# Optimization experiments

Measured on AMD Instinct MI355X. Metric: run time of the kernel, lower is better.

Reference implementation:

```python
import jax, jax.numpy as jnp
import numpy as np

B, N, D, H, C = 4, 512, 128, 128, 3


def setup_inputs() -> dict:
    key = jax.random.key(0)
    k1, k2, k3, k4, k5 = jax.random.split(key, 5)
    s1 = 1.0 / np.sqrt(2 * D)  # torch Linear default init scale (uniform bound); randn is fine for a numerics baseline
    s2 = 1.0 / np.sqrt(H)
    return {
        "h_dense": jax.random.normal(k1, (B, N, D), dtype=jnp.float32),
        "W1": jax.random.normal(k2, (H, 2 * D), dtype=jnp.float32) * s1,
        "b1": jax.random.normal(k3, (H,), dtype=jnp.float32) * s1,
        "W2": jax.random.normal(k4, (C, H), dtype=jnp.float32) * s2,
        "b2": jax.random.normal(k5, (C,), dtype=jnp.float32) * s2,
    }


def reference(h_dense, W1, b1, W2, b2):
    # Linear(concat(h_src, h_dst)) == h_src @ W1[:, :D].T + h_dst @ W1[:, D:].T + b1
    # which avoids materializing the (B, N, N, 2D) concat tensor (same math).
    d = h_dense.shape[-1]
    a = jnp.einsum("bnd,hd->bnh", h_dense, W1[:, :d])  # src projection (B, N, H)
    b = jnp.einsum("bnd,hd->bnh", h_dense, W1[:, d:])  # dst projection (B, N, H)
    pre = a[:, :, None, :] + b[:, None, :, :] + b1      # (B, N, N, H)
    act = jax.nn.silu(pre)
    logits = jnp.einsum("bijh,ch->bijc", act, W2) + b2  # (B, N, N, C)
    # symmetrize over the pair axes (dropout is identity in eval mode)
    return (logits + jnp.swapaxes(logits, 1, 2)) * 0.5
```

## Files before the change

### kernel.cpp

```cpp
#include <hip/hip_runtime.h>
#include <hip/hip_fp16.h>

#define B_ 4
#define N_ 512
#define D_ 128
#define H_ 128
#define C_ 3

#define NEG_LOG2E   (-1.4426950408889634f)
#define NEG_HALF_LN2 (-0.34657359027997264f)

#define PH   4
#define PHH  32
#define TROW 40

typedef _Float16 half8  __attribute__((ext_vector_type(8)));
typedef _Float16 half4v __attribute__((ext_vector_type(4)));

__device__ __forceinline__ float exp2_fast(float x) {
    return __builtin_amdgcn_exp2f(x);
}

__global__ __launch_bounds__(256) void proj_gemm(
    const float* __restrict__ hd, const float* __restrict__ W1,
    const float* __restrict__ b1, _Float16* __restrict__ At, _Float16* __restrict__ Bt)
{
    __shared__ float hsT[64][36];
    __shared__ float wt [64][68];
    const int m0      = blockIdx.x * 32;
    const int by      = blockIdx.y;
    const int halfSel = by >> 1;
    const int wrow0   = (by & 1) * 64;

    const int t  = threadIdx.x;
    const int r  = t >> 4, c4 = t & 15;
    const int tx = t & 15, ty = t >> 4;

    float acc[2][4] = {};

    for (int kc = 0; kc < 2; ++kc) {
        if (kc) __syncthreads();
        #pragma unroll
        for (int i = 0; i < 2; ++i) {
            const int m = r + 16 * i;
            float4 v = *(const float4*)&hd[(m0 + m) * D_ + kc * 64 + 4 * c4];
            hsT[4 * c4 + 0][m] = v.x; hsT[4 * c4 + 1][m] = v.y;
            hsT[4 * c4 + 2][m] = v.z; hsT[4 * c4 + 3][m] = v.w;
        }
        #pragma unroll
        for (int i = 0; i < 4; ++i) {
            const int o = r + 16 * i;
            float4 v = *(const float4*)&W1[(wrow0 + o) * (2 * D_) + halfSel * D_ + kc * 64 + 4 * c4];
            wt[4 * c4 + 0][o] = v.x; wt[4 * c4 + 1][o] = v.y;
            wt[4 * c4 + 2][o] = v.z; wt[4 * c4 + 3][o] = v.w;
        }
        __syncthreads();
        #pragma unroll 8
        for (int k = 0; k < 64; ++k) {
            float2 a  = *(const float2*)&hsT[k][2 * ty];
            float4 bv = *(const float4*)&wt [k][4 * tx];
            acc[0][0] = fmaf(a.x, bv.x, acc[0][0]); acc[0][1] = fmaf(a.x, bv.y, acc[0][1]);
            acc[0][2] = fmaf(a.x, bv.z, acc[0][2]); acc[0][3] = fmaf(a.x, bv.w, acc[0][3]);
            acc[1][0] = fmaf(a.y, bv.x, acc[1][0]); acc[1][1] = fmaf(a.y, bv.y, acc[1][1]);
            acc[1][2] = fmaf(a.y, bv.z, acc[1][2]); acc[1][3] = fmaf(a.y, bv.w, acc[1][3]);
        }
    }

    _Float16* dst = halfSel ? Bt : At;
    const int ocol = wrow0 + 4 * tx;
    float4 bias = make_float4(0.f, 0.f, 0.f, 0.f);
    if (!halfSel) bias = *(const float4*)&b1[ocol];
    #pragma unroll
    for (int i = 0; i < 2; ++i) {
        half4v o;
        o[0] = (_Float16)((acc[i][0] + bias.x) * NEG_LOG2E);
        o[1] = (_Float16)((acc[i][1] + bias.y) * NEG_LOG2E);
        o[2] = (_Float16)((acc[i][2] + bias.z) * NEG_LOG2E);
        o[3] = (_Float16)((acc[i][3] + bias.w) * NEG_LOG2E);
        *(half4v*)&dst[(m0 + 2 * ty + i) * H_ + ocol] = o;
    }
}

__global__ __launch_bounds__(256, 3) void pair_kernel(
    const _Float16* __restrict__ At, const _Float16* __restrict__ Bt,
    const float* __restrict__ W2, const float* __restrict__ b2,
    float* __restrict__ out)
{
    __shared__ __align__(16) _Float16 tiles[8][32 * TROW];
    const int T = N_ / 32;
    int tp = blockIdx.x;
    const int b = blockIdx.y;
    int I = 0;
    while (tp >= T - I) { tp -= T - I; ++I; }
    const int J = I + tp;

    const int tid = threadIdx.x;
    const int stile = tid >> 6;
    const int lane  = tid & 63;
    const int srow  = lane >> 1;
    const int scp   = lane & 1;
    const _Float16* gsrc = ((stile & 2) ? Bt : At)
        + (size_t)(b * N_ + ((stile & 1) ? J : I) * 32 + srow) * H_;
    _Float16* ybase = &tiles[stile][srow * TROW];
    _Float16* ebase = &tiles[stile + 4][srow * TROW];

    const int ti = tid >> 4, tj = tid & 15;
    float acc[4][3] = {};

    for (int ph = 0; ph < PH; ++ph) {
        if (ph) __syncthreads();
        #pragma unroll
        for (int q = 0; q < 2; ++q) {
            const int c = scp * 2 + q;
            half8 yv = *(const half8*)&gsrc[ph * PHH + c * 8];
            half8 ev;
            #pragma unroll
            for (int e = 0; e < 8; ++e)
                ev[e] = (_Float16)exp2_fast((float)yv[e]);
            *(half8*)&ybase[c * 8] = yv;
            *(half8*)&ebase[c * 8] = ev;
        }
        __syncthreads();

        #pragma unroll 2
        for (int c = 0; c < 4; ++c) {
            const int oI0 =  ti       * TROW + c * 8;
            const int oI1 = (ti + 16) * TROW + c * 8;
            const int oJ0 =  tj       * TROW + c * 8;
            const int oJ1 = (tj + 16) * TROW + c * 8;
            half8 yAI0 = *(const half8*)&tiles[0][oI0], yAI1 = *(const half8*)&tiles[0][oI1];
            half8 yAJ0 = *(const half8*)&tiles[1][oJ0], yAJ1 = *(const half8*)&tiles[1][oJ1];
            half8 yBI0 = *(const half8*)&tiles[2][oI0], yBI1 = *(const half8*)&tiles[2][oI1];
            half8 yBJ0 = *(const half8*)&tiles[3][oJ0], yBJ1 = *(const half8*)&tiles[3][oJ1];
            half8 eAI0 = *(const half8*)&tiles[4][oI0], eAI1 = *(const half8*)&tiles[4][oI1];
            half8 eAJ0 = *(const half8*)&tiles[5][oJ0], eAJ1 = *(const half8*)&tiles[5][oJ1];
            half8 eBI0 = *(const half8*)&tiles[6][oI0], eBI1 = *(const half8*)&tiles[6][oI1];
            half8 eBJ0 = *(const half8*)&tiles[7][oJ0], eBJ1 = *(const half8*)&tiles[7][oJ1];

            const int hb = ph * PHH + c * 8;
            float4 w0a = *(const float4*)&W2[hb],          w0b = *(const float4*)&W2[hb + 4];
            float4 w1a = *(const float4*)&W2[H_ + hb],     w1b = *(const float4*)&W2[H_ + hb + 4];
            float4 w2a = *(const float4*)&W2[2 * H_ + hb], w2b = *(const float4*)&W2[2 * H_ + hb + 4];
            const float w0[8] = {w0a.x, w0a.y, w0a.z, w0a.w, w0b.x, w0b.y, w0b.z, w0b.w};
            const float w1[8] = {w1a.x, w1a.y, w1a.z, w1a.w, w1b.x, w1b.y, w1b.z, w1b.w};
            const float w2[8] = {w2a.x, w2a.y, w2a.z, w2a.w, w2b.x, w2b.y, w2b.z, w2b.w};

            #define SILU4(p, yAIv, yBIv, eAIv, eBIv, yAJv, yBJv, eAJv, eBJv)      \
            {                                                                     \
                half8 y1 = (yAIv) + (yBJv);                                       \
                half8 y2 = (yAJv) + (yBIv);                                       \
                half8 e1 = (eAIv) * (eBJv);                                       \
                half8 e2 = (eAJv) * (eBIv);                                       \
                half8 d1 = e1 + (_Float16)1.0f;                                   \
                half8 d2 = e2 + (_Float16)1.0f;                                   \
                half8 pp = d1 * d2;                                               \
                half8 num = y1 * d2 + y2 * d1;                                    \
                _Pragma("unroll")                                                 \
                for (int e = 0; e < 8; ++e) {                                     \
                    const float s = (float)num[e]                                 \
                                  * __builtin_amdgcn_rcpf((float)pp[e]);          \
                    acc[p][0] = fmaf(s, w0[e], acc[p][0]);                        \
                    acc[p][1] = fmaf(s, w1[e], acc[p][1]);                        \
                    acc[p][2] = fmaf(s, w2[e], acc[p][2]);                        \
                }                                                                 \
            }
            SILU4(0, yAI0, yBI0, eAI0, eBI0, yAJ0, yBJ0, eAJ0, eBJ0)
            SILU4(1, yAI0, yBI0, eAI0, eBI0, yAJ1, yBJ1, eAJ1, eBJ1)
            SILU4(2, yAI1, yBI1, eAI1, eBI1, yAJ0, yBJ0, eAJ0, eBJ0)
            SILU4(3, yAI1, yBI1, eAI1, eBI1, yAJ1, yBJ1, eAJ1, eBJ1)
            #undef SILU4
        }
    }

    const float b20 = b2[0], b21 = b2[1], b22 = b2[2];
    #pragma unroll
    for (int p = 0; p < 4; ++p) {
        const int i = I * 32 + ti + (p >> 1) * 16;
        const int j = J * 32 + tj + (p & 1) * 16;
        const float o0 = fmaf(NEG_HALF_LN2, acc[p][0], b20);
        const float o1 = fmaf(NEG_HALF_LN2, acc[p][1], b21);
        const float o2 = fmaf(NEG_HALF_LN2, acc[p][2], b22);
        float* p1 = out + ((size_t)(b * N_ + i) * N_ + j) * C_;
        float* p2 = out + ((size_t)(b * N_ + j) * N_ + i) * C_;
        p1[0] = o0; p1[1] = o1; p1[2] = o2;
        p2[0] = o0; p2[1] = o1; p2[2] = o2;
    }
}

extern "C" void kernel_launch(void* const* d_in, const int* in_sizes, int n_in,
                              void* d_out, int out_size, void* d_ws, size_t ws_size,
                              hipStream_t stream) {
    const float* hd = (const float*)d_in[0];
    const float* W1 = (const float*)d_in[1];
    const float* b1 = (const float*)d_in[2];
    const float* W2 = (const float*)d_in[3];
    const float* b2 = (const float*)d_in[4];
    float* out = (float*)d_out;

    _Float16* At = (_Float16*)d_ws;
    _Float16* Bt = At + B_ * N_ * H_;

    proj_gemm<<<dim3((B_ * N_) / 32, 4), dim3(256), 0, stream>>>(hd, W1, b1, At, Bt);

    const int T = N_ / 32;
    pair_kernel<<<dim3(T * (T + 1) / 2, B_), dim3(256), 0, stream>>>(At, Bt, W2, b2, out);
}
```

Before: 48.00 us.

## Halve pair tile height to 16x32 and double block count

```diff
diff --git a/kernel.cpp b/kernel.cpp
--- a/kernel.cpp
+++ b/kernel.cpp
@@ -12,7 +12,7 @@
 
 #define PH   4
 #define PHH  32
-#define TROW 40
+#define SROW 40
 
 typedef _Float16 half8  __attribute__((ext_vector_type(8)));
 typedef _Float16 half4v __attribute__((ext_vector_type(4)));
@@ -86,56 +86,54 @@
     const float* __restrict__ W2, const float* __restrict__ b2,
     float* __restrict__ out)
 {
-    __shared__ __align__(16) _Float16 tiles[8][32 * TROW];
-    const int T = N_ / 32;
+    __shared__ __align__(16) _Float16 yt[96 * SROW];
+    __shared__ __align__(16) _Float16 et[96 * SROW];
+
+    const int b = blockIdx.y;
     int tp = blockIdx.x;
-    const int b = blockIdx.y;
-    int I = 0;
-    while (tp >= T - I) { tp -= T - I; ++I; }
-    const int J = I + tp;
+    int jt = 0;
+    while (tp >= 2 * jt + 2) { tp -= 2 * jt + 2; ++jt; }
+    const int it = tp;
+    const int I0 = it * 16, J0 = jt * 32;
 
     const int tid = threadIdx.x;
-    const int stile = tid >> 6;
-    const int lane  = tid & 63;
-    const int srow  = lane >> 1;
-    const int scp   = lane & 1;
-    const _Float16* gsrc = ((stile & 2) ? Bt : At)
-        + (size_t)(b * N_ + ((stile & 1) ? J : I) * 32 + srow) * H_;
-    _Float16* ybase = &tiles[stile][srow * TROW];
-    _Float16* ebase = &tiles[stile + 4][srow * TROW];
-
     const int ti = tid >> 4, tj = tid & 15;
-    float acc[4][3] = {};
+
+    float acc[2][3] = {};
 
     for (int ph = 0; ph < PH; ++ph) {
         if (ph) __syncthreads();
-        #pragma unroll
-        for (int q = 0; q < 2; ++q) {
-            const int c = scp * 2 + q;
-            half8 yv = *(const half8*)&gsrc[ph * PHH + c * 8];
+        for (int u = tid; u < 384; u += 256) {
+            const int row = u >> 2, c = u & 3;
+            const _Float16* base;
+            int gr;
+            if (row < 32)      { base = (row < 16) ? At : Bt; gr = I0 + (row & 15); }
+            else if (row < 64) { base = At; gr = J0 + (row - 32); }
+            else               { base = Bt; gr = J0 + (row - 64); }
+            half8 yv = *(const half8*)&base[(size_t)(b * N_ + gr) * H_ + ph * PHH + c * 8];
             half8 ev;
             #pragma unroll
             for (int e = 0; e < 8; ++e)
                 ev[e] = (_Float16)exp2_fast((float)yv[e]);
-            *(half8*)&ybase[c * 8] = yv;
-            *(half8*)&ebase[c * 8] = ev;
+            *(half8*)&yt[row * SROW + c * 8] = yv;
+            *(half8*)&et[row * SROW + c * 8] = ev;
         }
         __syncthreads();
 
         #pragma unroll 2
         for (int c = 0; c < 4; ++c) {
-            const int oI0 =  ti       * TROW + c * 8;
-            const int oI1 = (ti + 16) * TROW + c * 8;
-            const int oJ0 =  tj       * TROW + c * 8;
-            const int oJ1 = (tj + 16) * TROW + c * 8;
-            half8 yAI0 = *(const half8*)&tiles[0][oI0], yAI1 = *(const half8*)&tiles[0][oI1];
-            half8 yAJ0 = *(const half8*)&tiles[1][oJ0], yAJ1 = *(const half8*)&tiles[1][oJ1];
-            half8 yBI0 = *(const half8*)&tiles[2][oI0], yBI1 = *(const half8*)&tiles[2][oI1];
-            half8 yBJ0 = *(const half8*)&tiles[3][oJ0], yBJ1 = *(const half8*)&tiles[3][oJ1];
-            half8 eAI0 = *(const half8*)&tiles[4][oI0], eAI1 = *(const half8*)&tiles[4][oI1];
-            half8 eAJ0 = *(const half8*)&tiles[5][oJ0], eAJ1 = *(const half8*)&tiles[5][oJ1];
-            half8 eBI0 = *(const half8*)&tiles[6][oI0], eBI1 = *(const half8*)&tiles[6][oI1];
-            half8 eBJ0 = *(const half8*)&tiles[7][oJ0], eBJ1 = *(const half8*)&tiles[7][oJ1];
+            const int oAi  = ( 0 + ti) * SROW + c * 8;
+            const int oBi  = (16 + ti) * SROW + c * 8;
+            const int oAj0 = (32 + tj) * SROW + c * 8;
+            const int oAj1 = (48 + tj) * SROW + c * 8;
+            const int oBj0 = (64 + tj) * SROW + c * 8;
+            const int oBj1 = (80 + tj) * SROW + c * 8;
+            half8 yAi  = *(const half8*)&yt[oAi],  eAi  = *(const half8*)&et[oAi];
+            half8 yBi  = *(const half8*)&yt[oBi],  eBi  = *(const half8*)&et[oBi];
+            half8 yAj0 = *(const half8*)&yt[oAj0], eAj0 = *(const half8*)&et[oAj0];
+            half8 yAj1 = *(const half8*)&yt[oAj1], eAj1 = *(const half8*)&et[oAj1];
+            half8 yBj0 = *(const half8*)&yt[oBj0], eBj0 = *(const half8*)&et[oBj0];
+            half8 yBj1 = *(const half8*)&yt[oBj1], eBj1 = *(const half8*)&et[oBj1];
 
             const int hb = ph * PHH + c * 8;
             float4 w0a = *(const float4*)&W2[hb],          w0b = *(const float4*)&W2[hb + 4];
@@ -145,16 +143,19 @@
             const float w1[8] = {w1a.x, w1a.y, w1a.z, w1a.w, w1b.x, w1b.y, w1b.z, w1b.w};
             const float w2[8] = {w2a.x, w2a.y, w2a.z, w2a.w, w2b.x, w2b.y, w2b.z, w2b.w};
 
-            #define SILU4(p, yAIv, yBIv, eAIv, eBIv, yAJv, yBJv, eAJv, eBJv)      \
+            #define SILU2(p, yAj, yBj, eAj, eBj)                                  \
             {                                                                     \
-                half8 y1 = (yAIv) + (yBJv);                                       \
-                half8 y2 = (yAJv) + (yBIv);                                       \
-                half8 e1 = (eAIv) * (eBJv);                                       \
-                half8 e2 = (eAJv) * (eBIv);                                       \
+                half8 y1 = yAi + (yBj);                                           \
+                half8 y2 = (yAj) + yBi;                                           \
+                half8 e1 = eAi * (eBj);                                           \
+                half8 e2 = (eAj) * eBi;                                           \
                 half8 d1 = e1 + (_Float16)1.0f;                                   \
                 half8 d2 = e2 + (_Float16)1.0f;                                   \
                 half8 pp = d1 * d2;                                               \
-                half8 num = y1 * d2 + y2 * d1;                                    \
+                half8 t1 = y1 * d2;                                               \
+                half8 t2 = y2 * d1;                                               \
+                half8 num;                                                        \
+                { _Pragma("clang fp contract(off)") num = t1 + t2; }              \
                 _Pragma("unroll")                                                 \
                 for (int e = 0; e < 8; ++e) {                                     \
                     const float s = (float)num[e]                                 \
@@ -164,19 +165,17 @@
                     acc[p][2] = fmaf(s, w2[e], acc[p][2]);                        \
                 }                                                                 \
             }
-            SILU4(0, yAI0, yBI0, eAI0, eBI0, yAJ0, yBJ0, eAJ0, eBJ0)
-            SILU4(1, yAI0, yBI0, eAI0, eBI0, yAJ1, yBJ1, eAJ1, eBJ1)
-            SILU4(2, yAI1, yBI1, eAI1, eBI1, yAJ0, yBJ0, eAJ0, eBJ0)
-            SILU4(3, yAI1, yBI1, eAI1, eBI1, yAJ1, yBJ1, eAJ1, eBJ1)
-            #undef SILU4
+            SILU2(0, yAj0, yBj0, eAj0, eBj0)
+            SILU2(1, yAj1, yBj1, eAj1, eBj1)
+            #undef SILU2
         }
     }
 
     const float b20 = b2[0], b21 = b2[1], b22 = b2[2];
     #pragma unroll
-    for (int p = 0; p < 4; ++p) {
-        const int i = I * 32 + ti + (p >> 1) * 16;
-        const int j = J * 32 + tj + (p & 1) * 16;
+    for (int p = 0; p < 2; ++p) {
+        const int i = I0 + ti;
+        const int j = J0 + tj + p * 16;
         const float o0 = fmaf(NEG_HALF_LN2, acc[p][0], b20);
         const float o1 = fmaf(NEG_HALF_LN2, acc[p][1], b21);
         const float o2 = fmaf(NEG_HALF_LN2, acc[p][2], b22);
@@ -202,6 +201,5 @@
 
     proj_gemm<<<dim3((B_ * N_) / 32, 4), dim3(256), 0, stream>>>(hd, W1, b1, At, Bt);
 
-    const int T = N_ / 32;
-    pair_kernel<<<dim3(T * (T + 1) / 2, B_), dim3(256), 0, stream>>>(At, Bt, W2, b2, out);
-}
+    pair_kernel<<<dim3(272, B_), dim3(256), 0, stream>>>(At, Bt, W2, b2, out);
+}
```

New measurement: 50.14 us. 1.04x slower.
